# Kernel tuning notes

Hardware: AMD Instinct MI355X
Metric: run time of the kernel (lower is better)

Reference implementation:

```python
import jax, jax.numpy as jnp
import numpy as np

D_MODEL = 1024
NUM_HEADS = 16
HEAD_DIM = D_MODEL // NUM_HEADS


def setup_inputs() -> dict:
    key = jax.random.key(0)
    ks = jax.random.split(key, 5)
    x = jax.random.normal(ks[0], (2, 2048, D_MODEL), dtype=jnp.float32)
    s = 1.0 / np.sqrt(D_MODEL)
    # nn.Linear weight is [out, in]; y = x @ W.T
    Wq = jax.random.normal(ks[1], (D_MODEL, D_MODEL), dtype=jnp.float32) * s
    Wk = jax.random.normal(ks[2], (D_MODEL, D_MODEL), dtype=jnp.float32) * s
    Wv = jax.random.normal(ks[3], (D_MODEL, D_MODEL), dtype=jnp.float32) * s
    Wo = jax.random.normal(ks[4], (D_MODEL, D_MODEL), dtype=jnp.float32) * s
    return {"x": x, "Wq": Wq, "Wk": Wk, "Wv": Wv, "Wo": Wo}


def reference(x, Wq, Wk, Wv, Wo):
    b, s, d = x.shape
    h, hd = NUM_HEADS, HEAD_DIM
    # projections (Linear: x @ W.T), reshape to [b, h, s, hd]
    def proj(W):
        return (x @ W.T).reshape(b, s, h, hd).transpose(0, 2, 1, 3)
    Q, K, V = proj(Wq), proj(Wk), proj(Wv)
    # NOTE: original scales by 1/sqrt(d_model), not 1/sqrt(head_dim)
    scores = jnp.einsum('bhqd,bhkd->bhqk', Q, K) / jnp.sqrt(jnp.float32(d))
    attn = jax.nn.softmax(scores, axis=-1)
    ctx = jnp.einsum('bhqk,bhkd->bhqd', attn, V)
    ctx = ctx.transpose(0, 2, 1, 3).reshape(b, s, d)
    return ctx @ Wo.T
```

## Files before the change

kernel.cpp:

```cpp
#include <hip/hip_runtime.h>
#include <cstddef>
#include <cstdint>

#define SEQ 2048
#define DM 1024
#define NH 16
#define HD 64

typedef _Float16 f16;
typedef __attribute__((ext_vector_type(8))) _Float16 f16x8;
typedef __attribute__((ext_vector_type(4))) _Float16 f16x4;
typedef __attribute__((ext_vector_type(2))) _Float16 f16x2;
typedef __attribute__((ext_vector_type(4))) float f32x4;

__global__ __launch_bounds__(256) void cast_all(const float* __restrict__ x,
                                                const float* __restrict__ Wq,
                                                const float* __restrict__ Wk,
                                                const float* __restrict__ Wv,
                                                const float* __restrict__ Wo,
                                                f16* __restrict__ dst) {
  const int i = blockIdx.x * 256 + threadIdx.x;
  const float* src;
  int off;
  if (i < 1048576) {
    src = x; off = i;
  } else {
    const int j = i - 1048576;
    const int wsel = j >> 18;
    src = (wsel == 0) ? Wq : (wsel == 1) ? Wk : (wsel == 2) ? Wv : Wo;
    off = j & 262143;
  }
  const float4 v = ((const float4*)src)[off];
  f16x4 o = {(f16)v.x, (f16)v.y, (f16)v.z, (f16)v.w};
  ((f16x4*)dst)[i] = o;
}

__device__ __forceinline__ void gload16(const void* g, void* lds) {
  __builtin_amdgcn_global_load_lds((const __attribute__((address_space(1))) void*)g,
                                   (__attribute__((address_space(3))) void*)lds,
                                   16, 0, 0);
}

__device__ __forceinline__ void gemm_tile(const f16* __restrict__ A,
                                          const f16* __restrict__ B,
                                          f16* As, f16* Bs,
                                          int K, f32x4 acc[4][4]) {
  const int t = threadIdx.x;
  const int lane = t & 63;
  const int w = t >> 6;
  const int wm = (w & 1) << 6, wn = (w >> 1) << 6;
  const int srow = lane >> 2, scol = lane & 3;
  const int fr = lane & 15, q = lane >> 4;
  for (int k0 = 0; k0 < K; k0 += 32) {
    __syncthreads();
#pragma unroll
    for (int c = 0; c < 2; ++c) {
      const int chunk = (w << 1) + c;
      const int row = (chunk << 4) + srow;
      gload16(A + (size_t)row * K + k0 + (scol << 3), As + (chunk << 9));
      gload16(B + (size_t)row * K + k0 + (scol << 3), Bs + (chunk << 9));
    }
    __syncthreads();
    f16x8 af[4], bfr[4];
#pragma unroll
    for (int i = 0; i < 4; ++i)
      af[i] = *(const f16x8*)(As + (wm + (i << 4) + fr) * 32 + (q << 3));
#pragma unroll
    for (int j = 0; j < 4; ++j)
      bfr[j] = *(const f16x8*)(Bs + (wn + (j << 4) + fr) * 32 + (q << 3));
#pragma unroll
    for (int i = 0; i < 4; ++i)
#pragma unroll
      for (int j = 0; j < 4; ++j)
        acc[i][j] = __builtin_amdgcn_mfma_f32_16x16x32_f16(af[i], bfr[j],
                                                           acc[i][j], 0, 0, 0);
  }
}

#define QSCALE 0.04508422003f
__global__ __launch_bounds__(256) void gemm_qkv(
    const f16* __restrict__ xb, const f16* __restrict__ Wqb,
    const f16* __restrict__ Wkb, const f16* __restrict__ Wvb,
    f16* __restrict__ Qb, f16* __restrict__ Kb, f16* __restrict__ Vtg) {
  __shared__ f16 smem[16384];
  f16* As = smem;
  f16* Bs = smem + 4096;
  const int which = blockIdx.x >> 3;
  const int bn = (blockIdx.x & 7) << 7;
  const int bm = blockIdx.y << 7;
  const f16* B = (which == 0) ? Wqb : (which == 1) ? Wkb : Wvb;
  f32x4 acc[4][4] = {};
  gemm_tile(xb + (size_t)bm * DM, B + (size_t)bn * DM, As, Bs, DM, acc);
  const int lane = threadIdx.x & 63, w = threadIdx.x >> 6;
  const int wm = (w & 1) << 6, wn = (w >> 1) << 6;
  const int col = lane & 15, q = lane >> 4;
  if (which < 2) {
    f16* C = (which == 0) ? Qb : Kb;
    const float sc = (which == 0) ? QSCALE : 1.0f;
#pragma unroll
    for (int i = 0; i < 4; ++i) {
      const int m = bm + wm + (i << 4) + (q << 2);
#pragma unroll
      for (int j = 0; j < 4; ++j) {
        const int n = bn + wn + (j << 4) + col;
#pragma unroll
        for (int r = 0; r < 4; ++r)
          C[(size_t)(m + r) * DM + n] = (f16)(acc[i][j][r] * sc);
      }
    }
  } else {
    __syncthreads();
#pragma unroll
    for (int i = 0; i < 4; ++i) {
      const int m0 = wm + (i << 4) + (q << 2);
      const int cm = m0 >> 3, sub = (m0 >> 2) & 1;
#pragma unroll
      for (int j = 0; j < 4; ++j) {
        const int nl = wn + (j << 4) + col;
        f16x4 o = {(f16)acc[i][j][0], (f16)acc[i][j][1],
                   (f16)acc[i][j][2], (f16)acc[i][j][3]};
        *(f16x4*)(smem + nl * 128 +
                  ((cm ^ (nl & 15) ^ ((nl >> 4) & 3)) << 3) + (sub << 2)) = o;
      }
    }
    __syncthreads();
    const int b = bm >> 11, sb = bm & 2047;
    const int d = threadIdx.x & 63;
#pragma unroll
    for (int step = 0; step < 16; ++step) {
      const int idx = (threadIdx.x >> 6) + (step << 2);
      const int hh = idx >> 5, s4 = idx & 31;
      const int nl = (hh << 6) + d;
      const int cm = s4 >> 1, sub = s4 & 1;
      const f16x4 v = *(const f16x4*)(smem + nl * 128 +
                                      ((cm ^ (nl & 15) ^ ((nl >> 4) & 3)) << 3) +
                                      (sub << 2));
      const int bh = (b << 4) + (bn >> 6) + hh;
      const int sg = sb + (s4 << 2);
      const size_t flat = ((size_t)bh << 17) + ((size_t)(sg >> 6) << 12) +
                          ((s4 & 15) << 8) + (d << 2);
      *(f16x4*)(Vtg + flat) = v;
    }
  }
}

__global__ __launch_bounds__(256) void gemm_out(const f16* __restrict__ Ab,
                                                const f16* __restrict__ Wob,
                                                float* __restrict__ out) {
  __shared__ f16 As[128 * 32];
  __shared__ f16 Bs[128 * 32];
  const int bn = blockIdx.x << 7, bm = blockIdx.y << 7;
  f32x4 acc[4][4] = {};
  gemm_tile(Ab + (size_t)bm * DM, Wob + (size_t)bn * DM, As, Bs, DM, acc);
  const int lane = threadIdx.x & 63, w = threadIdx.x >> 6;
  const int wm = (w & 1) << 6, wn = (w >> 1) << 6;
  const int col = lane & 15, q = lane >> 4;
#pragma unroll
  for (int i = 0; i < 4; ++i) {
    const int m = bm + wm + (i << 4) + (q << 2);
#pragma unroll
    for (int j = 0; j < 4; ++j) {
      const int n = bn + wn + (j << 4) + col;
#pragma unroll
      for (int r = 0; r < 4; ++r)
        out[(size_t)(m + r) * DM + n] = acc[i][j][r];
    }
  }
}

__global__ __launch_bounds__(256, 2) void attn_mfma(const f16* __restrict__ Qb,
                                                    const f16* __restrict__ Kb,
                                                    const f16* __restrict__ Vtg,
                                                    f16* __restrict__ Ctx) {
  __shared__ f16 smem[8192];
  const int t = threadIdx.x, lane = t & 63, w = t >> 6;
  const int fr = lane & 15, quad = lane >> 4;
  const int i = blockIdx.x;
  const int j = i >> 3;
  const int bh = ((i & 7) << 2) + (j >> 4);
  const int qt16 = j & 15;
  const int b = bh >> 4, h = bh & 15;

  const size_t qrow0 = (size_t)b * SEQ + qt16 * 128 + w * 32;

  f16x8 Qf[2][2];
#pragma unroll
  for (int qt = 0; qt < 2; ++qt)
#pragma unroll
    for (int hf = 0; hf < 2; ++hf)
      Qf[qt][hf] = *(const f16x8*)(Qb + (qrow0 + qt * 16 + fr) * DM + h * HD +
                                   hf * 32 + (quad << 3));

  const int krow = lane >> 2, kkc = lane & 3;
  const f16* Kg = Kb + ((size_t)b * SEQ + 16 * w + krow) * DM + h * HD + (kkc << 3);
  const int cwr = ((krow >> 1) << 3) | ((krow & 1) << 2) | (((krow >> 1) + kkc) & 3);
  const int wofs = (w << 9) + (cwr << 3);
  const int crd = ((fr >> 1) << 3) | ((fr & 1) << 2) | (((fr >> 1) + quad) & 3);

  const f16* Vg = Vtg + ((size_t)bh << 17) + (quad << 8) + (fr << 2);

  f16x8 kreg[2];
  f16x4 va[4][4], vb[4][4];
  auto loadK = [&](int kt) {
#pragma unroll
    for (int hf = 0; hf < 2; ++hf)
      kreg[hf] = *(const f16x8*)(Kg + (size_t)kt * 64 * DM + hf * 32);
  };
  auto loadV = [&](int kt, f16x4 (&vr)[4][4]) {
#pragma unroll
    for (int kc = 0; kc < 4; ++kc)
#pragma unroll
      for (int dt = 0; dt < 4; ++dt)
        vr[dt][kc] = *(const f16x4*)(Vg + kt * 4096 + (kc << 10) + (dt << 6));
  };

  f32x4 acc[2][4] = {};
  float lacc[2] = {0.f, 0.f};

  f16* img0 = smem;
  f16* img1 = smem + 4096;

  loadK(0);
  loadV(0, va);
  *(f16x8*)(img0 + wofs) = kreg[0];
  *(f16x8*)(img0 + wofs + 2048) = kreg[1];

  auto body = [&](int kt, f16x4 (&vcur)[4][4], f16x4 (&vnxt)[4][4],
                  f16* imgR, f16* imgW) {
    __syncthreads();
    if (kt < 31) {
      loadK(kt + 1);
      loadV(kt + 1, vnxt);
    }
    f16x8 Kf[4][2];
#pragma unroll
    for (int mt = 0; mt < 4; ++mt)
#pragma unroll
      for (int hf = 0; hf < 2; ++hf)
        Kf[mt][hf] = *(const f16x8*)(imgR + (crd << 3) + hf * 2048 + (mt << 9));

    f16x4 pf[2][4];
#pragma unroll
    for (int qt = 0; qt < 2; ++qt) {
      f32x4 z[4] = {};
#pragma unroll
      for (int mt = 0; mt < 4; ++mt) {
        z[mt] = __builtin_amdgcn_mfma_f32_16x16x32_f16(Kf[mt][0], Qf[qt][0],
                                                       z[mt], 0, 0, 0);
        z[mt] = __builtin_amdgcn_mfma_f32_16x16x32_f16(Kf[mt][1], Qf[qt][1],
                                                       z[mt], 0, 0, 0);
      }
#pragma unroll
      for (int mt = 0; mt < 4; ++mt) {
        const float p0 = __builtin_amdgcn_exp2f(z[mt][0]);
        const float p1 = __builtin_amdgcn_exp2f(z[mt][1]);
        const float p2 = __builtin_amdgcn_exp2f(z[mt][2]);
        const float p3 = __builtin_amdgcn_exp2f(z[mt][3]);
        lacc[qt] += (p0 + p1) + (p2 + p3);
        const f16x2 lo = __builtin_bit_cast(f16x2, __builtin_amdgcn_cvt_pkrtz(p0, p1));
        const f16x2 hi = __builtin_bit_cast(f16x2, __builtin_amdgcn_cvt_pkrtz(p2, p3));
        f16x4 pv; pv.x = lo.x; pv.y = lo.y; pv.z = hi.x; pv.w = hi.y;
        pf[qt][mt] = pv;
      }
    }

#pragma unroll
    for (int dt = 0; dt < 4; ++dt)
#pragma unroll
      for (int kc = 0; kc < 4; ++kc)
#pragma unroll
        for (int qt = 0; qt < 2; ++qt)
          acc[qt][dt] = __builtin_amdgcn_mfma_f32_16x16x16f16(vcur[dt][kc],
                                                              pf[qt][kc],
                                                              acc[qt][dt], 0, 0, 0);
    if (kt < 31) {
      *(f16x8*)(imgW + wofs) = kreg[0];
      *(f16x8*)(imgW + wofs + 2048) = kreg[1];
    }
  };

  for (int kt = 0; kt < 32; kt += 2) {
    body(kt, va, vb, img0, img1);
    body(kt + 1, vb, va, img1, img0);
  }

  float inv[2];
#pragma unroll
  for (int qt = 0; qt < 2; ++qt) {
    float l = lacc[qt];
    l += __shfl_xor(l, 16);
    l += __shfl_xor(l, 32);
    inv[qt] = __builtin_amdgcn_rcpf(l);
  }

  __syncthreads();
  f16* T = smem + (w << 11);
#pragma unroll
  for (int qt = 0; qt < 2; ++qt)
#pragma unroll
    for (int dt = 0; dt < 4; ++dt) {
      f16x4 o = {(f16)(acc[qt][dt][0] * inv[qt]), (f16)(acc[qt][dt][1] * inv[qt]),
                 (f16)(acc[qt][dt][2] * inv[qt]), (f16)(acc[qt][dt][3] * inv[qt])};
      *(f16x4*)(T + (qt * 16 + fr) * 64 + dt * 16 + (quad << 2)) = o;
    }
#pragma unroll
  for (int p = 0; p < 4; ++p) {
    const int ql = p * 8 + (lane >> 3);
    const f16x8 v = *(const f16x8*)(T + ql * 64 + ((lane & 7) << 3));
    *(f16x8*)(Ctx + (qrow0 + ql) * DM + h * HD + ((lane & 7) << 3)) = v;
  }
}

extern "C" void kernel_launch(void* const* d_in, const int* in_sizes, int n_in,
                              void* d_out, int out_size, void* d_ws, size_t ws_size,
                              hipStream_t stream) {
  const float* x  = (const float*)d_in[0];
  const float* Wq = (const float*)d_in[1];
  const float* Wk = (const float*)d_in[2];
  const float* Wv = (const float*)d_in[3];
  const float* Wo = (const float*)d_in[4];

  char* ws = (char*)d_ws;
  f16* xb  = (f16*)(ws);
  f16* Wb  = (f16*)(ws + (8u << 20));
  f16* Wqb = Wb;
  f16* Wkb = Wb + 1048576;
  f16* Wvb = Wb + 2097152;
  f16* Wob = Wb + 3145728;
  f16* Qb  = (f16*)(ws + (16u << 20));
  f16* Kb  = (f16*)(ws + (24u << 20));
  f16* Vtg = (f16*)(ws + (32u << 20));
  f16* Ctx = (f16*)(ws + (40u << 20));

  cast_all<<<8192, 256, 0, stream>>>(x, Wq, Wk, Wv, Wo, xb);

  gemm_qkv<<<dim3(24, 32), 256, 0, stream>>>(xb, Wqb, Wkb, Wvb, Qb, Kb, Vtg);
  attn_mfma<<<dim3(2 * NH * (SEQ / 128)), 256, 0, stream>>>(Qb, Kb, Vtg, Ctx);
  gemm_out<<<dim3(8, 32), 256, 0, stream>>>(Ctx, Wob, (float*)d_out);
}
```

Baseline: 194.7 us.

## Stage K and V tiles into LDS via direct global-to-LDS loads

The attention kernel no longer stages K through registers or keeps V tiles in register arrays. Both are now loaded straight into double-buffered LDS images with gload16, and each wave reads its V fragments as f16x8 from LDS. The V-transpose producer writes a new interleaved layout so these 16-byte loads map straight onto MFMA operands, and the K source column is rotated to keep the LDS swizzle. The aim is to cut VGPR pressure and register-staging stores so loads overlap compute. The cost is twice the LDS per block, which may lower occupancy, plus extra LDS read traffic for V.

```diff
diff --git a/kernel.cpp b/kernel.cpp
--- a/kernel.cpp
+++ b/kernel.cpp
@@ -138,7 +138,9 @@
       const int bh = (b << 4) + (bn >> 6) + hh;
       const int sg = sb + (s4 << 2);
       const size_t flat = ((size_t)bh << 17) + ((size_t)(sg >> 6) << 12) +
-                          ((s4 & 15) << 8) + (d << 2);
+                          ((size_t)(d >> 4) << 10) + (((size_t)(s4 >> 3) & 1) << 9) +
+                          (((size_t)s4 & 3) << 7) + (((size_t)d & 15) << 3) +
+                          (((size_t)(s4 >> 2) & 1) << 2);
       *(f16x4*)(Vtg + flat) = v;
     }
   }
@@ -172,7 +174,7 @@
                                                     const f16* __restrict__ Kb,
                                                     const f16* __restrict__ Vtg,
                                                     f16* __restrict__ Ctx) {
-  __shared__ f16 smem[8192];
+  __shared__ f16 smem[16384];
   const int t = threadIdx.x, lane = t & 63, w = t >> 6;
   const int fr = lane & 15, quad = lane >> 4;
   const int i = blockIdx.x;
@@ -191,97 +193,94 @@
       Qf[qt][hf] = *(const f16x8*)(Qb + (qrow0 + qt * 16 + fr) * DM + h * HD +
                                    hf * 32 + (quad << 3));
 
-  const int krow = lane >> 2, kkc = lane & 3;
+  const int krow = lane >> 2;
+  const int kkc = ((lane & 3) - (lane >> 3)) & 3;
   const f16* Kg = Kb + ((size_t)b * SEQ + 16 * w + krow) * DM + h * HD + (kkc << 3);
-  const int cwr = ((krow >> 1) << 3) | ((krow & 1) << 2) | (((krow >> 1) + kkc) & 3);
-  const int wofs = (w << 9) + (cwr << 3);
+  const f16* Vg = Vtg + ((size_t)bh << 17) + (((w << 7) + lane) << 3);
+
   const int crd = ((fr >> 1) << 3) | ((fr & 1) << 2) | (((fr >> 1) + quad) & 3);
 
-  const f16* Vg = Vtg + ((size_t)bh << 17) + (quad << 8) + (fr << 2);
-
-  f16x8 kreg[2];
-  f16x4 va[4][4], vb[4][4];
-  auto loadK = [&](int kt) {
+  f16* K0 = smem;
+  f16* K1 = smem + 4096;
+  f16* V0 = smem + 8192;
+  f16* V1 = smem + 12288;
+
+  auto stage = [&](int kt, f16* Kimg, f16* Vimg) {
 #pragma unroll
     for (int hf = 0; hf < 2; ++hf)
-      kreg[hf] = *(const f16x8*)(Kg + (size_t)kt * 64 * DM + hf * 32);
-  };
-  auto loadV = [&](int kt, f16x4 (&vr)[4][4]) {
-#pragma unroll
-    for (int kc = 0; kc < 4; ++kc)
-#pragma unroll
-      for (int dt = 0; dt < 4; ++dt)
-        vr[dt][kc] = *(const f16x4*)(Vg + kt * 4096 + (kc << 10) + (dt << 6));
+      gload16(Kg + (size_t)kt * 64 * DM + hf * 32,
+              Kimg + (hf << 11) + (w << 9));
+#pragma unroll
+    for (int c = 0; c < 2; ++c)
+      gload16(Vg + kt * 4096 + (c << 9), Vimg + (w << 10) + (c << 9));
   };
 
   f32x4 acc[2][4] = {};
   float lacc[2] = {0.f, 0.f};
 
-  f16* img0 = smem;
-  f16* img1 = smem + 4096;
-
-  loadK(0);
-  loadV(0, va);
-  *(f16x8*)(img0 + wofs) = kreg[0];
-  *(f16x8*)(img0 + wofs + 2048) = kreg[1];
-
-  auto body = [&](int kt, f16x4 (&vcur)[4][4], f16x4 (&vnxt)[4][4],
-                  f16* imgR, f16* imgW) {
-    __syncthreads();
-    if (kt < 31) {
-      loadK(kt + 1);
-      loadV(kt + 1, vnxt);
-    }
+  stage(0, K0, V0);
+
+  auto body = [&](int kt, f16* KR, f16* VR, f16* KW, f16* VW) {
+    __syncthreads();
+    if (kt < 31) stage(kt + 1, KW, VW);
+
     f16x8 Kf[4][2];
 #pragma unroll
     for (int mt = 0; mt < 4; ++mt)
 #pragma unroll
       for (int hf = 0; hf < 2; ++hf)
-        Kf[mt][hf] = *(const f16x8*)(imgR + (crd << 3) + hf * 2048 + (mt << 9));
+        Kf[mt][hf] = *(const f16x8*)(KR + (crd << 3) + (hf << 11) + (mt << 9));
+    f16x8 Vf[4][2];
+#pragma unroll
+    for (int dt = 0; dt < 4; ++dt)
+#pragma unroll
+      for (int kp = 0; kp < 2; ++kp)
+        Vf[dt][kp] = *(const f16x8*)(VR + (((dt << 1) | kp) << 9) +
+                                     (quad << 7) + (fr << 3));
+
+    f32x4 z[2][4] = {};
+#pragma unroll
+    for (int hf = 0; hf < 2; ++hf)
+#pragma unroll
+      for (int qt = 0; qt < 2; ++qt)
+#pragma unroll
+        for (int mt = 0; mt < 4; ++mt)
+          z[qt][mt] = __builtin_amdgcn_mfma_f32_16x16x32_f16(Kf[mt][hf], Qf[qt][hf],
+                                                             z[qt][mt], 0, 0, 0);
 
     f16x4 pf[2][4];
 #pragma unroll
-    for (int qt = 0; qt < 2; ++qt) {
-      f32x4 z[4] = {};
+    for (int qt = 0; qt < 2; ++qt)
 #pragma unroll
       for (int mt = 0; mt < 4; ++mt) {
-        z[mt] = __builtin_amdgcn_mfma_f32_16x16x32_f16(Kf[mt][0], Qf[qt][0],
-                                                       z[mt], 0, 0, 0);
-        z[mt] = __builtin_amdgcn_mfma_f32_16x16x32_f16(Kf[mt][1], Qf[qt][1],
-                                                       z[mt], 0, 0, 0);
-      }
-#pragma unroll
-      for (int mt = 0; mt < 4; ++mt) {
-        const float p0 = __builtin_amdgcn_exp2f(z[mt][0]);
-        const float p1 = __builtin_amdgcn_exp2f(z[mt][1]);
-        const float p2 = __builtin_amdgcn_exp2f(z[mt][2]);
-        const float p3 = __builtin_amdgcn_exp2f(z[mt][3]);
+        const float p0 = __builtin_amdgcn_exp2f(z[qt][mt][0]);
+        const float p1 = __builtin_amdgcn_exp2f(z[qt][mt][1]);
+        const float p2 = __builtin_amdgcn_exp2f(z[qt][mt][2]);
+        const float p3 = __builtin_amdgcn_exp2f(z[qt][mt][3]);
         lacc[qt] += (p0 + p1) + (p2 + p3);
         const f16x2 lo = __builtin_bit_cast(f16x2, __builtin_amdgcn_cvt_pkrtz(p0, p1));
         const f16x2 hi = __builtin_bit_cast(f16x2, __builtin_amdgcn_cvt_pkrtz(p2, p3));
         f16x4 pv; pv.x = lo.x; pv.y = lo.y; pv.z = hi.x; pv.w = hi.y;
         pf[qt][mt] = pv;
       }
-    }
-
-#pragma unroll
-    for (int dt = 0; dt < 4; ++dt)
-#pragma unroll
-      for (int kc = 0; kc < 4; ++kc)
+
+#pragma unroll
+    for (int kc = 0; kc < 4; ++kc)
+#pragma unroll
+      for (int dt = 0; dt < 4; ++dt) {
+        const f16x8 v8 = Vf[dt][kc >> 1];
+        const f16x4 vh = (kc & 1) ? __builtin_shufflevector(v8, v8, 4, 5, 6, 7)
+                                  : __builtin_shufflevector(v8, v8, 0, 1, 2, 3);
 #pragma unroll
         for (int qt = 0; qt < 2; ++qt)
-          acc[qt][dt] = __builtin_amdgcn_mfma_f32_16x16x16f16(vcur[dt][kc],
-                                                              pf[qt][kc],
+          acc[qt][dt] = __builtin_amdgcn_mfma_f32_16x16x16f16(vh, pf[qt][kc],
                                                               acc[qt][dt], 0, 0, 0);
-    if (kt < 31) {
-      *(f16x8*)(imgW + wofs) = kreg[0];
-      *(f16x8*)(imgW + wofs + 2048) = kreg[1];
-    }
+      }
   };
 
   for (int kt = 0; kt < 32; kt += 2) {
-    body(kt, va, vb, img0, img1);
-    body(kt + 1, vb, va, img1, img0);
+    body(kt, K0, V0, K1, V1);
+    body(kt + 1, K1, V1, K0, V0);
   }
 
   float inv[2];
```

After: 195.5 us. Within noise of the previous version (+0.4%).
